# Kernel optimization log

Measured on AMD Instinct MI355X. Metric: run time of the kernel, lower is better.

## Reference

```python
import jax, jax.numpy as jnp
import numpy as np

KS = 3      # kernel_size
PAD = 1     # padding
GROUPS = 4

def _patches(a, H, W):
    # a: [B, C, H+2*PAD, W+2*PAD] -> [B, C, H, W, KS, KS]
    return jnp.stack([
        jnp.stack([a[:, :, i:i + H, j:j + W] for j in range(KS)], axis=-1)
        for i in range(KS)], axis=-2)

def setup_inputs() -> dict:
    key = jax.random.key(0)
    ks = jax.random.split(key, 7)
    B, Cin, Cout, H, W = 8, 256, 256, 64, 64
    std = np.sqrt(2.0 / Cout)  # kaiming fan_out
    return {
        "x": jax.random.normal(ks[0], (B, Cin, H, W), jnp.float32),
        "y": jax.random.normal(ks[1], (B, Cin, H, W), jnp.float32),
        "wq": jax.random.normal(ks[2], (Cout, Cin), jnp.float32) * std,
        "wk": jax.random.normal(ks[3], (Cout, Cin), jnp.float32) * std,
        "wv": jax.random.normal(ks[4], (Cout, Cin), jnp.float32) * std,
        "rel_h": jax.random.normal(ks[5], (Cout // 2, 1, 1, KS, 1), jnp.float32),
        "rel_w": jax.random.normal(ks[6], (Cout // 2, 1, 1, 1, KS), jnp.float32),
    }

def reference(x, y, wq, wk, wv, rel_h, rel_w):
    B, _, H, W = x.shape
    Cout = wq.shape[0]
    half = Cout // 2
    xp = jnp.pad(x, ((0, 0), (0, 0), (PAD, PAD), (PAD, PAD)))
    q = jnp.einsum('oi,bihw->bohw', wq, y)          # [B,Cout,H,W]
    k = jnp.einsum('oi,bihw->bohw', wk, xp)         # [B,Cout,H+2,W+2]
    v = jnp.einsum('oi,bihw->bohw', wv, xp)
    kp = _patches(k, H, W)                          # [B,Cout,H,W,KS,KS]
    vp = _patches(v, H, W)
    kp = jnp.concatenate([kp[:, :half] + rel_h[None], kp[:, half:] + rel_w[None]], axis=1)
    cg = Cout // GROUPS
    kp = kp.reshape(B, GROUPS, cg, H, W, KS * KS)
    vp = vp.reshape(B, GROUPS, cg, H, W, KS * KS)
    qg = q.reshape(B, GROUPS, cg, H, W, 1)
    attn = jax.nn.softmax(qg * kp, axis=-1)         # per-channel softmax over window
    out = jnp.einsum('bnchwk,bnchwk->bnchw', attn, vp)
    return out.reshape(B, Cout, H, W)
```

## Files before the change

kernel.cpp:

```cpp
#include <hip/hip_runtime.h>
#include <hip/hip_bf16.h>
#include <stdint.h>

typedef __attribute__((ext_vector_type(8))) short short8;
typedef __attribute__((ext_vector_type(4))) float floatx4;
typedef __attribute__((ext_vector_type(4))) unsigned int uintx4;
typedef __attribute__((ext_vector_type(2))) unsigned int uintx2;
typedef unsigned int u32;

#define HH 64
#define WW 64
#define HWSZ 4096
#define BB 8
#define CIN 256
#define COUT 256
#define NTOT 32768

#define GLL16(g, l)                                                            \
    __builtin_amdgcn_global_load_lds(                                          \
        (const __attribute__((address_space(1))) u32*)(const void*)(g),        \
        (__attribute__((address_space(3))) u32*)(void*)(l), 16, 0, 0)

__device__ __forceinline__ unsigned short f2b(float f) {
    union { float f; unsigned int u; } v; v.f = f;
    unsigned int r = v.u + 0x7FFFu + ((v.u >> 16) & 1u);
    return (unsigned short)(r >> 16);
}
__device__ __forceinline__ float b2f(unsigned short h) {
    union { unsigned int u; float f; } v; v.u = ((unsigned int)h) << 16;
    return v.f;
}
__device__ __forceinline__ unsigned int pk2(float lo, float hi) {
    unsigned int r;
    asm("v_cvt_pk_bf16_f32 %0, %1, %2" : "=v"(r) : "v"(lo), "v"(hi));
    return r;
}

__global__ void wcast(const float* __restrict__ wq, const float* __restrict__ wk,
                      const float* __restrict__ wv,
                      unsigned short* __restrict__ wqb, unsigned short* __restrict__ wkb,
                      unsigned short* __restrict__ wvb) {
    int idx = blockIdx.x * 256 + threadIdx.x;
    wqb[idx] = f2b(wq[idx]);
    wkb[idx] = f2b(wk[idx]);
    wvb[idx] = f2b(wv[idx]);
}

__global__ __launch_bounds__(256)
void gemm_qkv(const unsigned short* __restrict__ wqb, const unsigned short* __restrict__ wkb,
              const unsigned short* __restrict__ wvb,
              const float* __restrict__ xf, const float* __restrict__ yf,
              unsigned short* __restrict__ Qb, unsigned short* __restrict__ Kb,
              unsigned short* __restrict__ Vb) {
    __shared__ unsigned short lA[2][128 * 32];
    __shared__ unsigned short lB[2][128 * 32];

    int z = blockIdx.z;
    const unsigned short* Wb = (z == 0) ? wqb : (z == 1) ? wkb : wvb;
    const float* In = (z == 0) ? yf : xf;
    unsigned short* Out = (z == 0) ? Qb : (z == 1) ? Kb : Vb;

    int n0 = blockIdx.x * 128;
    int m0 = blockIdx.y * 128;
    int b  = n0 >> 12;
    int p0 = n0 & 4095;
    int t = threadIdx.x;
    int lane = t & 63;
    int wave = t >> 6;
    int quad = lane >> 4;
    int l16 = lane & 15;
    int wm = (wave >> 1) * 64;
    int wn = (wave & 1) * 64;

    int sA0 = t >> 2;
    int cch = (t & 3) * 8;
    const unsigned short* gA0 = Wb + (size_t)(m0 + sA0) * CIN + cch;
    const unsigned short* gA1 = Wb + (size_t)(m0 + sA0 + 64) * CIN + cch;

    int ng = (t & 31) * 4;
    int kq = (t >> 5) * 4;
    const float* gB = In + ((size_t)b * CIN + kq) * HWSZ + p0 + ng;
    int sbase = t & 31;
    int wr_idx[4];
    #pragma unroll
    for (int j = 0; j < 4; ++j) {
        int s = j * 32 + sbase;
        wr_idx[j] = s * 32 + (((kq >> 3) ^ ((s >> 1) & 3)) << 3) + (kq & 4);
    }

    int rB = (wn >> 2) + l16;
    int swzr = (rB >> 1) & 3;
    int rd_off = rB * 32 + ((quad ^ swzr) << 3);

    floatx4 acc[4][4];
    #pragma unroll
    for (int mi = 0; mi < 4; ++mi)
        #pragma unroll
        for (int ni = 0; ni < 4; ++ni)
            acc[mi][ni] = (floatx4){0.f, 0.f, 0.f, 0.f};

    floatx4 pb[2][4];
    #pragma unroll
    for (int bs = 0; bs < 2; ++bs)
        #pragma unroll
        for (int i = 0; i < 4; ++i)
            pb[bs][i] = *(const floatx4*)(gB + (size_t)(bs * 32 + i) * HWSZ);

    #pragma unroll
    for (int it = 0; it < 4; ++it) {
        int k0 = it * 64;
        #pragma unroll
        for (int bs = 0; bs < 2; ++bs) {
            int ko = k0 + bs * 32;
            unsigned short* dA = lA[bs] + wave * 512;
            GLL16(gA0 + ko, dA);
            GLL16(gA1 + ko, dA + 2048);
        }
        floatx4 nb[2][4];
        if (it < 3) {
            #pragma unroll
            for (int bs = 0; bs < 2; ++bs)
                #pragma unroll
                for (int i = 0; i < 4; ++i)
                    nb[bs][i] = *(const floatx4*)(gB + (size_t)(k0 + 64 + bs * 32 + i) * HWSZ);
        }
        #pragma unroll
        for (int bs = 0; bs < 2; ++bs) {
            #pragma unroll
            for (int j = 0; j < 4; ++j) {
                unsigned int d0 = pk2(pb[bs][0][j], pb[bs][1][j]);
                unsigned int d1 = pk2(pb[bs][2][j], pb[bs][3][j]);
                *(uintx2*)(lB[bs] + wr_idx[j]) = (uintx2){d0, d1};
            }
        }
        __syncthreads();

        #pragma unroll
        for (int bs = 0; bs < 2; ++bs) {
            short8 af[4], bf[4];
            #pragma unroll
            for (int mi = 0; mi < 4; ++mi)
                af[mi] = *(const short8*)(lA[bs] + (wm + mi * 16 + l16) * 32 + quad * 8);
            #pragma unroll
            for (int ni = 0; ni < 4; ++ni)
                bf[ni] = *(const short8*)(lB[bs] + rd_off + ni * 1024);
            #pragma unroll
            for (int mi = 0; mi < 4; ++mi)
                #pragma unroll
                for (int ni = 0; ni < 4; ++ni)
                    acc[mi][ni] = __builtin_amdgcn_mfma_f32_16x16x32_bf16(af[mi], bf[ni], acc[mi][ni], 0, 0, 0);
        }
        __syncthreads();

        if (it < 3) {
            #pragma unroll
            for (int bs = 0; bs < 2; ++bs)
                #pragma unroll
                for (int i = 0; i < 4; ++i)
                    pb[bs][i] = nb[bs][i];
        }
    }

    int colb = n0 + wn + 4 * l16;
    #pragma unroll
    for (int mi = 0; mi < 4; ++mi) {
        #pragma unroll
        for (int r = 0; r < 4; ++r) {
            int row = m0 + wm + mi * 16 + quad * 4 + r;
            unsigned int lo = (unsigned int)f2b(acc[mi][0][r]) | ((unsigned int)f2b(acc[mi][1][r]) << 16);
            unsigned int hi = (unsigned int)f2b(acc[mi][2][r]) | ((unsigned int)f2b(acc[mi][3][r]) << 16);
            *(uintx2*)(Out + (size_t)row * NTOT + colb) = (uintx2){lo, hi};
        }
    }
}

__global__ __launch_bounds__(256)
void attn(const unsigned short* __restrict__ Q,
          const unsigned short* __restrict__ K,
          const unsigned short* __restrict__ V,
          const float* __restrict__ rel_h,
          const float* __restrict__ rel_w,
          float* __restrict__ out) {
    int gid = blockIdx.x * 256 + threadIdx.x;
    int w8 = gid & 7;
    int w0 = w8 << 3;
    int h = (gid >> 3) & 63;
    int c = (gid >> 9) & 255;
    int b = gid >> 17;

    size_t nb = (size_t)c * NTOT + (size_t)b * HWSZ;
    const unsigned short* Kp = K + nb;
    const unsigned short* Vp = V + nb;

    short8 qr = *(const short8*)(Q + nb + h * 64 + w0);

    bool use_h = (c < 128);
    float rel3[3];
    if (use_h) {
        rel3[0] = rel_h[c * 3 + 0]; rel3[1] = rel_h[c * 3 + 1]; rel3[2] = rel_h[c * 3 + 2];
    } else {
        int cc = c - 128;
        rel3[0] = rel_w[cc * 3 + 0]; rel3[1] = rel_w[cc * 3 + 1]; rel3[2] = rel_w[cc * 3 + 2];
    }
    float rr[9];
    #pragma unroll
    for (int r = 0; r < 3; ++r)
        #pragma unroll
        for (int j = 0; j < 3; ++j)
            rr[r * 3 + j] = use_h ? rel3[r] : rel3[j];

    int e0 = (w0 > 0) ? w0 - 1 : 0;
    int e9 = (w0 < 56) ? w0 + 8 : 63;
    bool okL = (w0 > 0);
    bool okR = (w0 < 56);

    float kb[3][10], vb[3][10];
    #pragma unroll
    for (int r = 0; r < 3; ++r) {
        int ihr = h + r - 1;
        bool rok = (unsigned)ihr < 64u;
        int ihc = ihr < 0 ? 0 : (ihr > 63 ? 63 : ihr);
        int ro = ihc * 64;
        short8 km = *(const short8*)(Kp + ro + w0);
        short8 vm = *(const short8*)(Vp + ro + w0);
        float ke0 = b2f(Kp[ro + e0]), ve0 = b2f(Vp[ro + e0]);
        float ke9 = b2f(Kp[ro + e9]), ve9 = b2f(Vp[ro + e9]);
        #pragma unroll
        for (int i = 0; i < 8; ++i) {
            kb[r][i + 1] = rok ? b2f((unsigned short)km[i]) : 0.f;
            vb[r][i + 1] = rok ? b2f((unsigned short)vm[i]) : 0.f;
        }
        bool ok0 = rok && okL;
        bool ok9 = rok && okR;
        kb[r][0] = ok0 ? ke0 : 0.f;  vb[r][0] = ok0 ? ve0 : 0.f;
        kb[r][9] = ok9 ? ke9 : 0.f;  vb[r][9] = ok9 ? ve9 : 0.f;
    }

    float q[8];
    #pragma unroll
    for (int i = 0; i < 8; ++i) q[i] = b2f((unsigned short)qr[i]);

    float ov[8];
    #pragma unroll
    for (int wi = 0; wi < 8; ++wi) {
        float qv = q[wi];
        float lg[9];
        #pragma unroll
        for (int r = 0; r < 3; ++r)
            #pragma unroll
            for (int j = 0; j < 3; ++j)
                lg[r * 3 + j] = qv * (kb[r][wi + j] + rr[r * 3 + j]);
        float m = lg[0];
        #pragma unroll
        for (int t2 = 1; t2 < 9; ++t2) m = fmaxf(m, lg[t2]);
        float s = 0.f, o = 0.f;
        #pragma unroll
        for (int r = 0; r < 3; ++r)
            #pragma unroll
            for (int j = 0; j < 3; ++j) {
                float e = __expf(lg[r * 3 + j] - m);
                s += e;
                o += e * vb[r][wi + j];
            }
        ov[wi] = o * __builtin_amdgcn_rcpf(s);
    }

    size_t oi = ((size_t)b * COUT + c) * HWSZ + h * 64 + w0;
    *(floatx4*)(out + oi)     = (floatx4){ ov[0], ov[1], ov[2], ov[3] };
    *(floatx4*)(out + oi + 4) = (floatx4){ ov[4], ov[5], ov[6], ov[7] };
}

extern "C" void kernel_launch(void* const* d_in, const int* in_sizes, int n_in,
                              void* d_out, int out_size, void* d_ws, size_t ws_size,
                              hipStream_t stream) {
    const float* x = (const float*)d_in[0];
    const float* y = (const float*)d_in[1];
    const float* wq = (const float*)d_in[2];
    const float* wk = (const float*)d_in[3];
    const float* wv = (const float*)d_in[4];
    const float* rel_h = (const float*)d_in[5];
    const float* rel_w = (const float*)d_in[6];
    float* out = (float*)d_out;

    char* ws = (char*)d_ws;
    unsigned short* wqb = (unsigned short*)(ws + 33554432);
    unsigned short* wkb = (unsigned short*)(ws + 33554432 + 131072);
    unsigned short* wvb = (unsigned short*)(ws + 33554432 + 262144);
    unsigned short* Qb  = (unsigned short*)(ws + 33947648);
    unsigned short* Kb  = (unsigned short*)(ws + 33947648 + 16777216);
    unsigned short* Vb  = (unsigned short*)(ws + 33947648 + 33554432);

    wcast<<<256, 256, 0, stream>>>(wq, wk, wv, wqb, wkb, wvb);
    gemm_qkv<<<dim3(256, 2, 3), 256, 0, stream>>>(wqb, wkb, wvb, x, y, Qb, Kb, Vb);
    attn<<<4096, 256, 0, stream>>>(Qb, Kb, Vb, rel_h, rel_w, out);
}
```

Measured before the change: 152.2 us.

## Software-pipeline QKV GEMM K-loop with double-buffered LDS and explicit waitcnts

```diff
diff --git a/kernel.cpp b/kernel.cpp
--- a/kernel.cpp
+++ b/kernel.cpp
@@ -62,7 +62,7 @@
 
     int n0 = blockIdx.x * 128;
     int m0 = blockIdx.y * 128;
-    int b  = n0 >> 12;
+    int bb = n0 >> 12;
     int p0 = n0 & 4095;
     int t = threadIdx.x;
     int lane = t & 63;
@@ -72,15 +72,16 @@
     int wm = (wave >> 1) * 64;
     int wn = (wave & 1) * 64;
 
-    int sA0 = t >> 2;
-    int cch = (t & 3) * 8;
-    const unsigned short* gA0 = Wb + (size_t)(m0 + sA0) * CIN + cch;
-    const unsigned short* gA1 = Wb + (size_t)(m0 + sA0 + 64) * CIN + cch;
-
-    int ng = (t & 31) * 4;
+    int rA = t >> 2;
+    int qA = t & 3;
+    int cchA = 8 * (qA ^ ((rA >> 1) & 3));
+    const unsigned short* gA0 = Wb + (size_t)(m0 + rA) * CIN + cchA;
+    const unsigned short* gA1 = gA0 + (size_t)64 * CIN;
+
+    int sbase = t & 31;
+    int ng = sbase * 4;
     int kq = (t >> 5) * 4;
-    const float* gB = In + ((size_t)b * CIN + kq) * HWSZ + p0 + ng;
-    int sbase = t & 31;
+    const float* gB = In + ((size_t)bb * CIN + kq) * HWSZ + p0 + ng;
     int wr_idx[4];
     #pragma unroll
     for (int j = 0; j < 4; ++j) {
@@ -88,9 +89,11 @@
         wr_idx[j] = s * 32 + (((kq >> 3) ^ ((s >> 1) & 3)) << 3) + (kq & 4);
     }
 
-    int rB = (wn >> 2) + l16;
-    int swzr = (rB >> 1) & 3;
-    int rd_off = rB * 32 + ((quad ^ swzr) << 3);
+    int swzA = (l16 >> 1) & 3;
+    int rBr = (wn >> 2) + l16;
+    int swzB = (rBr >> 1) & 3;
+    int rdA = (wm + l16) * 32 + ((quad ^ swzA) << 3);
+    int rdB = rBr * 32 + ((quad ^ swzB) << 3);
 
     floatx4 acc[4][4];
     #pragma unroll
@@ -99,65 +102,68 @@
         for (int ni = 0; ni < 4; ++ni)
             acc[mi][ni] = (floatx4){0.f, 0.f, 0.f, 0.f};
 
-    floatx4 pb[2][4];
-    #pragma unroll
-    for (int bs = 0; bs < 2; ++bs)
-        #pragma unroll
-        for (int i = 0; i < 4; ++i)
-            pb[bs][i] = *(const floatx4*)(gB + (size_t)(bs * 32 + i) * HWSZ);
-
-    #pragma unroll
-    for (int it = 0; it < 4; ++it) {
-        int k0 = it * 64;
-        #pragma unroll
-        for (int bs = 0; bs < 2; ++bs) {
-            int ko = k0 + bs * 32;
-            unsigned short* dA = lA[bs] + wave * 512;
-            GLL16(gA0 + ko, dA);
-            GLL16(gA1 + ko, dA + 2048);
-        }
-        floatx4 nb[2][4];
-        if (it < 3) {
-            #pragma unroll
-            for (int bs = 0; bs < 2; ++bs)
-                #pragma unroll
-                for (int i = 0; i < 4; ++i)
-                    nb[bs][i] = *(const floatx4*)(gB + (size_t)(k0 + 64 + bs * 32 + i) * HWSZ);
-        }
-        #pragma unroll
-        for (int bs = 0; bs < 2; ++bs) {
+    floatx4 bl[2][4];
+
+    #pragma unroll
+    for (int i = 0; i < 4; ++i)
+        bl[0][i] = *(const floatx4*)(gB + (size_t)i * HWSZ);
+    __builtin_amdgcn_sched_barrier(0);
+    GLL16(gA0, lA[0] + wave * 512);
+    GLL16(gA1, lA[0] + wave * 512 + 2048);
+    __builtin_amdgcn_sched_barrier(0);
+    #pragma unroll
+    for (int i = 0; i < 4; ++i)
+        bl[1][i] = *(const floatx4*)(gB + (size_t)(32 + i) * HWSZ);
+    asm volatile("s_waitcnt vmcnt(6)" ::: "memory");
+    #pragma unroll
+    for (int j = 0; j < 4; ++j) {
+        unsigned int d0 = pk2(bl[0][0][j], bl[0][1][j]);
+        unsigned int d1 = pk2(bl[0][2][j], bl[0][3][j]);
+        *(uintx2*)(lB[0] + wr_idx[j]) = (uintx2){d0, d1};
+    }
+    asm volatile("s_waitcnt vmcnt(4) lgkmcnt(0)" ::: "memory");
+    __builtin_amdgcn_s_barrier();
+    __builtin_amdgcn_sched_barrier(0);
+
+    #pragma unroll
+    for (int it = 0; it < 8; ++it) {
+        if (it < 7) {
+            GLL16(gA0 + (it + 1) * 32, lA[(it + 1) & 1] + wave * 512);
+            GLL16(gA1 + (it + 1) * 32, lA[(it + 1) & 1] + wave * 512 + 2048);
+        }
+        __builtin_amdgcn_sched_barrier(0);
+        if (it < 6) {
+            #pragma unroll
+            for (int i = 0; i < 4; ++i)
+                bl[it & 1][i] = *(const floatx4*)(gB + (size_t)((it + 2) * 32 + i) * HWSZ);
+        }
+
+        short8 af[4], bf[4];
+        #pragma unroll
+        for (int mi = 0; mi < 4; ++mi)
+            af[mi] = *(const short8*)(lA[it & 1] + rdA + mi * 512);
+        #pragma unroll
+        for (int ni = 0; ni < 4; ++ni)
+            bf[ni] = *(const short8*)(lB[it & 1] + rdB + ni * 1024);
+        #pragma unroll
+        for (int mi = 0; mi < 4; ++mi)
+            #pragma unroll
+            for (int ni = 0; ni < 4; ++ni)
+                acc[mi][ni] = __builtin_amdgcn_mfma_f32_16x16x32_bf16(af[mi], bf[ni], acc[mi][ni], 0, 0, 0);
+
+        if (it < 7) {
+            if (it < 6) { asm volatile("s_waitcnt vmcnt(6)" ::: "memory"); }
+            else        { asm volatile("s_waitcnt vmcnt(2)" ::: "memory"); }
             #pragma unroll
             for (int j = 0; j < 4; ++j) {
-                unsigned int d0 = pk2(pb[bs][0][j], pb[bs][1][j]);
-                unsigned int d1 = pk2(pb[bs][2][j], pb[bs][3][j]);
-                *(uintx2*)(lB[bs] + wr_idx[j]) = (uintx2){d0, d1};
+                unsigned int d0 = pk2(bl[(it + 1) & 1][0][j], bl[(it + 1) & 1][1][j]);
+                unsigned int d1 = pk2(bl[(it + 1) & 1][2][j], bl[(it + 1) & 1][3][j]);
+                *(uintx2*)(lB[(it + 1) & 1] + wr_idx[j]) = (uintx2){d0, d1};
             }
-        }
-        __syncthreads();
-
-        #pragma unroll
-        for (int bs = 0; bs < 2; ++bs) {
-            short8 af[4], bf[4];
-            #pragma unroll
-            for (int mi = 0; mi < 4; ++mi)
-                af[mi] = *(const short8*)(lA[bs] + (wm + mi * 16 + l16) * 32 + quad * 8);
-            #pragma unroll
-            for (int ni = 0; ni < 4; ++ni)
-                bf[ni] = *(const short8*)(lB[bs] + rd_off + ni * 1024);
-            #pragma unroll
-            for (int mi = 0; mi < 4; ++mi)
-                #pragma unroll
-                for (int ni = 0; ni < 4; ++ni)
-                    acc[mi][ni] = __builtin_amdgcn_mfma_f32_16x16x32_bf16(af[mi], bf[ni], acc[mi][ni], 0, 0, 0);
-        }
-        __syncthreads();
-
-        if (it < 3) {
-            #pragma unroll
-            for (int bs = 0; bs < 2; ++bs)
-                #pragma unroll
-                for (int i = 0; i < 4; ++i)
-                    pb[bs][i] = nb[bs][i];
+            if (it < 6) { asm volatile("s_waitcnt vmcnt(4) lgkmcnt(0)" ::: "memory"); }
+            else        { asm volatile("s_waitcnt vmcnt(0) lgkmcnt(0)" ::: "memory"); }
+            __builtin_amdgcn_s_barrier();
+            __builtin_amdgcn_sched_barrier(0);
         }
     }
 
```

New measurement: 153.4 us. Within noise of the previous version (+0.8%).
